# Optimization experiments

Hardware: AMD Instinct MI355X
Metric: run time of the kernel (lower is better)

Reference implementation:

```python
import jax, jax.numpy as jnp
import numpy as np

M = 4096          # number of quadrature points
D_OBS = 64        # number of observation directions
KVALS = (0.5, 1.0, 1.5, 2.0)   # wavenumbers (init k_values)
N_ITER = 5        # Born iterations
C = 1.0 / (4.0 * np.pi)        # Green's function constant


def setup_inputs() -> dict:
    key = jax.random.key(0)
    k1, k2, k3, k4 = jax.random.split(key, 4)
    pts = jax.random.normal(k1, (M, 3), dtype=jnp.float32)
    weights = jax.random.uniform(k2, (M,), dtype=jnp.float32)
    V = jax.random.normal(k3, (M,), dtype=jnp.float32)
    obs_dirs = jax.random.normal(k4, (D_OBS, 3), dtype=jnp.float32)
    obs_dirs = obs_dirs / jnp.linalg.norm(obs_dirs, axis=1, keepdims=True)
    return {"V": V, "obs_dirs": obs_dirs, "pts": pts, "weights": weights}


def reference(V, obs_dirs, pts, weights):
    dtype = V.dtype
    dhat = jnp.array([0.0, 0.0, 1.0], dtype=dtype)  # default incident_dir, already unit
    dot_d = pts @ dhat                               # [M]
    r2 = jnp.sum(pts * pts, axis=1)                  # [M]

    # Pairwise distances; faithful to D2 = r2_i + r2_j - 2 pts_i . pts_j
    D2 = r2[:, None] + r2[None, :] - 2.0 * (pts @ pts.T)   # [M, M]
    D = jnp.sqrt(jnp.clip(D2, 1e-12, None))
    invD = 1.0 / jnp.clip(D, 1e-6, None)
    idx = jnp.arange(M)
    invD = jnp.where(idx[:, None] == idx[None, :], jnp.zeros((), dtype), invD)
    scale = C * invD                                  # [M, M]

    VW = V * weights                                  # [M]
    Q = pts @ obs_dirs.T                              # [M, D_OBS]

    outs = []
    for k in KVALS:
        # Green's-function kernel (same across Born iterations for fixed k)
        Gr = scale * jnp.cos(k * D)                   # [M, M]
        Gi = scale * jnp.sin(k * D)                   # [M, M]

        # incident plane wave psi0 = exp(i k r.dhat)
        p0r = jnp.cos(k * dot_d)
        p0i = jnp.sin(k * dot_d)
        pr, pi_ = p0r, p0i
        for _ in range(N_ITER):
            ar = pr * VW
            ai = pi_ * VW
            pr = p0r + (Gr @ ar - Gi @ ai)
            pi_ = p0i + (Gr @ ai + Gi @ ar)

        # far-field amplitude: f(k, obs) = -C * sum_j w_j V_j psi_j exp(-i k pts_j.obs)
        phr = jnp.cos(-k * Q)                         # [M, D_OBS]
        phi = jnp.sin(-k * Q)
        zr = V * pr                                   # [M]
        zi = V * pi_
        ir = zr[:, None] * phr - zi[:, None] * phi    # [M, D_OBS]
        ii = zr[:, None] * phi + zi[:, None] * phr
        fr = jnp.sum(ir * weights[:, None], axis=0)   # [D_OBS]
        fi = jnp.sum(ii * weights[:, None], axis=0)
        outs.append(jnp.stack([-C * fr, -C * fi], axis=-1))  # [D_OBS, 2]

    return jnp.stack(outs, axis=0)                    # [len(KVALS), D_OBS, 2]
```

## Files before the change

### kernel.cpp

```cpp
#include <hip/hip_runtime.h>


#define MM 4096
#define NK 4
#define CGREEN 0.07957747154594767f

#define OFF_VW   49152
#define OFF_P0R  53248
#define OFF_P0I  69632
#define OFF_YR   86016
#define OFF_YI   102400
#define OFF_PART 118784
#define NCHUNK 128
#define PART_FLOATS (NCHUNK * 8 * MM)
#define WS_NEED_PART ((size_t)(OFF_PART + PART_FLOATS) * 4)

typedef float f2 __attribute__((ext_vector_type(2)));

__global__ __launch_bounds__(256) void init_k(const float* __restrict__ V,
                                              const float* __restrict__ pts,
                                              const float* __restrict__ w,
                                              float* __restrict__ ws) {
#pragma clang fp contract(off)
    int i = blockIdx.x * 256 + threadIdx.x;
    float x = pts[3 * i], y = pts[3 * i + 1], z = pts[3 * i + 2];
    float cvw = CGREEN * (V[i] * w[i]);
    float xx = x * x, yy = y * y, zz = z * z;
    float r2 = (xx + yy) + zz;
    float* cp = ws + i * 12;
    cp[0] = x; cp[1] = y; cp[2] = z; cp[3] = r2;
    ws[OFF_VW + i] = cvw;
#pragma unroll
    for (int n = 0; n < NK; n++) {
        float kk = 0.5f * (float)(n + 1);
        float s, c;
        sincosf(kk * z, &s, &c);
        ws[OFF_P0R + n * MM + i] = c;
        ws[OFF_P0I + n * MM + i] = s;
        cp[4 + n] = cvw * c;
        cp[8 + n] = cvw * s;
        ws[OFF_YR + n * MM + i] = 0.0f;
        ws[OFF_YI + n * MM + i] = 0.0f;
    }
}

__device__ __forceinline__ f2 cmul(f2 a, f2 b) {
    f2 r;
    r.x = fmaf(a.x, b.x, -(a.y * b.y));
    r.y = fmaf(a.x, b.y,  (a.y * b.x));
    return r;
}

__device__ __forceinline__ void body(float rx, float ry, float rz, float rr2,
                                     int rowg, int jg,
                                     float4 A, float4 R, float4 I,
                                     f2 acc[4]) {
    float d2;
    {
#pragma clang fp contract(off)
        float dot = fmaf(rz, A.z, fmaf(ry, A.y, rx * A.x));
        float r2s = rr2 + A.w;
        float twod = 2.0f * dot;
        d2 = r2s - twod;
    }
    d2 = fmaxf(d2, 1e-12f);
    float invD = __builtin_amdgcn_rsqf(d2);
    float D = d2 * invD;
    float scale = (rowg == jg) ? 0.0f : invD;
    float s1, c1;
    __sincosf(0.5f * D, &s1, &c1);
    f2 cs1 = {c1, s1};
    f2 cs2 = cmul(cs1, cs1);
    f2 cs3 = cmul(cs2, cs1);
    f2 cs4 = cmul(cs2, cs2);
    {
        f2 ri = {R.x, I.x}, sw = {-I.x, R.x};
        f2 t = cs1.x * ri; t += cs1.y * sw; acc[0] += scale * t;
    }
    {
        f2 ri = {R.y, I.y}, sw = {-I.y, R.y};
        f2 t = cs2.x * ri; t += cs2.y * sw; acc[1] += scale * t;
    }
    {
        f2 ri = {R.z, I.z}, sw = {-I.z, R.z};
        f2 t = cs3.x * ri; t += cs3.y * sw; acc[2] += scale * t;
    }
    {
        f2 ri = {R.w, I.w}, sw = {-I.w, R.w};
        f2 t = cs4.x * ri; t += cs4.y * sw; acc[3] += scale * t;
    }
}

template <int C, bool USE_PART>
__global__ __launch_bounds__(256) void matvec_k(float* __restrict__ ws) {
    constexpr int TC = MM / C;
    const int chunk = blockIdx.x;
    const int rg = blockIdx.y;
    const int r0 = rg * 256 + threadIdx.x;
    const float4 row0 = *(const float4*)&ws[r0 * 12];
    f2 acc[4];
#pragma unroll
    for (int i = 0; i < 4; i++) { acc[i].x = 0.0f; acc[i].y = 0.0f; }
    const int jg0 = chunk * TC;
    const float* colbase = ws + (size_t)jg0 * 12;
#pragma unroll 4
    for (int j = 0; j < TC; j++) {
        const float4* cp = (const float4*)(colbase + j * 12);
        float4 A = cp[0], R = cp[1], I = cp[2];
        body(row0.x, row0.y, row0.z, row0.w, r0, jg0 + j, A, R, I, acc);
    }
    if (USE_PART) {
        f2* part2 = (f2*)(ws + OFF_PART);
#pragma unroll
        for (int n = 0; n < NK; n++)
            part2[(size_t)(chunk * 4 + n) * MM + r0] = acc[n];
    } else {
        float* yr = ws + OFF_YR;
        float* yi = ws + OFF_YI;
#pragma unroll
        for (int n = 0; n < NK; n++) {
            atomicAdd(&yr[n * MM + r0], acc[n].x);
            atomicAdd(&yi[n * MM + r0], acc[n].y);
        }
    }
}

template <int C>
__global__ __launch_bounds__(64) void reduce_update_k(float* __restrict__ ws) {
    int tid = blockIdx.x * 64 + threadIdx.x;
    int row = tid & (MM - 1);
    int n = tid >> 12;
    const f2* part2 = (const f2*)(ws + OFF_PART);
    f2 s[8];
#pragma unroll
    for (int u = 0; u < 8; u++) { s[u].x = 0.0f; s[u].y = 0.0f; }
    for (int c = 0; c < C; c += 8) {
#pragma unroll
        for (int u = 0; u < 8; u++)
            s[u] += part2[(size_t)((c + u) * 4 + n) * MM + row];
    }
    f2 t = ((s[0] + s[1]) + (s[2] + s[3])) + ((s[4] + s[5]) + (s[6] + s[7]));
    float cvw = ws[OFF_VW + row];
    float pr = ws[OFF_P0R + n * MM + row] + t.x;
    float pi = ws[OFF_P0I + n * MM + row] + t.y;
    ws[row * 12 + 4 + n] = cvw * pr;
    ws[row * 12 + 8 + n] = cvw * pi;
}

__global__ __launch_bounds__(256) void update_fallback_k(float* __restrict__ ws) {
    int i = blockIdx.x * 256 + threadIdx.x;
    float cvw = ws[OFF_VW + i];
#pragma unroll
    for (int n = 0; n < NK; n++) {
        float pr = ws[OFF_P0R + n * MM + i] + ws[OFF_YR + n * MM + i];
        float pi = ws[OFF_P0I + n * MM + i] + ws[OFF_YI + n * MM + i];
        ws[i * 12 + 4 + n] = cvw * pr;
        ws[i * 12 + 8 + n] = cvw * pi;
        ws[OFF_YR + n * MM + i] = 0.0f;
        ws[OFF_YI + n * MM + i] = 0.0f;
    }
}

__global__ __launch_bounds__(256) void far_k(const float* __restrict__ obs,
                                             const float* __restrict__ ws,
                                             float* __restrict__ out) {
    int kidx = blockIdx.x >> 6;
    int d = blockIdx.x & 63;
    float kk = 0.5f * (float)(kidx + 1);
    float ox = obs[3 * d], oy = obs[3 * d + 1], oz = obs[3 * d + 2];
    float fr = 0.0f, fi = 0.0f;
    for (int j = threadIdx.x; j < MM; j += 256) {
        const float* c = ws + j * 12;
        float q = fmaf(c[2], oz, fmaf(c[1], oy, c[0] * ox));
        float ar = c[4 + kidx], ai = c[8 + kidx];
        float s, co;
        __sincosf(kk * q, &s, &co);
        fr += fmaf(ar, co,  ai * s);
        fi += fmaf(ai, co, -ar * s);
    }
#pragma unroll
    for (int off = 32; off > 0; off >>= 1) {
        fr += __shfl_down(fr, off);
        fi += __shfl_down(fi, off);
    }
    __shared__ float red[4][2];
    int wave = threadIdx.x >> 6;
    if ((threadIdx.x & 63) == 0) { red[wave][0] = fr; red[wave][1] = fi; }
    __syncthreads();
    if (threadIdx.x == 0) {
        fr = red[0][0] + red[1][0] + red[2][0] + red[3][0];
        fi = red[0][1] + red[1][1] + red[2][1] + red[3][1];
        out[(kidx * 64 + d) * 2 + 0] = -fr;
        out[(kidx * 64 + d) * 2 + 1] = -fi;
    }
}

extern "C" void kernel_launch(void* const* d_in, const int* in_sizes, int n_in,
                              void* d_out, int out_size, void* d_ws, size_t ws_size,
                              hipStream_t stream) {
    const float* V   = (const float*)d_in[0];
    const float* obs = (const float*)d_in[1];
    const float* pts = (const float*)d_in[2];
    const float* w   = (const float*)d_in[3];
    float* ws  = (float*)d_ws;
    float* out = (float*)d_out;

    init_k<<<16, 256, 0, stream>>>(V, pts, w, ws);
    if (ws_size >= WS_NEED_PART) {
        for (int it = 0; it < 5; it++) {
            matvec_k<NCHUNK, true><<<dim3(NCHUNK, 16), 256, 0, stream>>>(ws);
            reduce_update_k<NCHUNK><<<256, 64, 0, stream>>>(ws);
        }
    } else {
        for (int it = 0; it < 5; it++) {
            matvec_k<64, false><<<dim3(64, 16), 256, 0, stream>>>(ws);
            update_fallback_k<<<16, 256, 0, stream>>>(ws);
        }
    }
    far_k<<<256, 256, 0, stream>>>(obs, ws, out);
}
```

Baseline: 223.8 us.

## Process two rows per thread with packed f2 math and hardware sin/cos

Each matvec thread now handles two rows (r0 and r0+256), so every loaded column record is reused twice, and the grid is halved in the row dimension. Distance and harmonic computations are written in packed two-wide vectors so the compiler can emit packed FMA instructions. The sincos call is replaced by the raw hardware sin/cos builtins on a revolution-scaled argument. This cuts column loads and per-element instruction count, at the cost of more registers, fewer blocks, and possible accuracy loss from hardware sin/cos on larger arguments.

```diff
diff --git a/kernel.cpp b/kernel.cpp
--- a/kernel.cpp
+++ b/kernel.cpp
@@ -4,6 +4,7 @@
 #define MM 4096
 #define NK 4
 #define CGREEN 0.07957747154594767f
+#define INV2PI 0.15915494309189535f
 
 #define OFF_VW   49152
 #define OFF_P0R  53248
@@ -16,6 +17,10 @@
 #define WS_NEED_PART ((size_t)(OFF_PART + PART_FLOATS) * 4)
 
 typedef float f2 __attribute__((ext_vector_type(2)));
+
+__device__ __forceinline__ f2 vfma(f2 a, f2 b, f2 c) {
+    f2 r; r.x = fmaf(a.x, b.x, c.x); r.y = fmaf(a.y, b.y, c.y); return r;
+}
 
 __global__ __launch_bounds__(256) void init_k(const float* __restrict__ V,
                                               const float* __restrict__ pts,
@@ -44,83 +49,95 @@
     }
 }
 
-__device__ __forceinline__ f2 cmul(f2 a, f2 b) {
-    f2 r;
-    r.x = fmaf(a.x, b.x, -(a.y * b.y));
-    r.y = fmaf(a.x, b.y,  (a.y * b.x));
-    return r;
-}
-
-__device__ __forceinline__ void body(float rx, float ry, float rz, float rr2,
-                                     int rowg, int jg,
-                                     float4 A, float4 R, float4 I,
-                                     f2 acc[4]) {
-    float d2;
+__device__ __forceinline__ void body_col2(f2 rx, f2 ry, f2 rz, f2 rr2,
+                                          int r0, int r1, int jg,
+                                          float4 A, float4 R, float4 I,
+                                          f2 acc0[4], f2 acc1[4]) {
+    f2 d2;
     {
 #pragma clang fp contract(off)
-        float dot = fmaf(rz, A.z, fmaf(ry, A.y, rx * A.x));
-        float r2s = rr2 + A.w;
-        float twod = 2.0f * dot;
+        f2 m; m.x = rx.x * A.x; m.y = rx.y * A.x;
+        m = vfma(ry, (f2){A.y, A.y}, m);
+        m = vfma(rz, (f2){A.z, A.z}, m);
+        f2 r2s = rr2 + A.w;
+        f2 twod = 2.0f * m;
         d2 = r2s - twod;
     }
-    d2 = fmaxf(d2, 1e-12f);
-    float invD = __builtin_amdgcn_rsqf(d2);
-    float D = d2 * invD;
-    float scale = (rowg == jg) ? 0.0f : invD;
-    float s1, c1;
-    __sincosf(0.5f * D, &s1, &c1);
-    f2 cs1 = {c1, s1};
-    f2 cs2 = cmul(cs1, cs1);
-    f2 cs3 = cmul(cs2, cs1);
-    f2 cs4 = cmul(cs2, cs2);
-    {
-        f2 ri = {R.x, I.x}, sw = {-I.x, R.x};
-        f2 t = cs1.x * ri; t += cs1.y * sw; acc[0] += scale * t;
-    }
-    {
-        f2 ri = {R.y, I.y}, sw = {-I.y, R.y};
-        f2 t = cs2.x * ri; t += cs2.y * sw; acc[1] += scale * t;
-    }
-    {
-        f2 ri = {R.z, I.z}, sw = {-I.z, R.z};
-        f2 t = cs3.x * ri; t += cs3.y * sw; acc[2] += scale * t;
-    }
-    {
-        f2 ri = {R.w, I.w}, sw = {-I.w, R.w};
-        f2 t = cs4.x * ri; t += cs4.y * sw; acc[3] += scale * t;
-    }
+    d2.x = fmaxf(d2.x, 1e-12f);
+    d2.y = fmaxf(d2.y, 1e-12f);
+    float ia = __builtin_amdgcn_rsqf(d2.x);
+    float ib = __builtin_amdgcn_rsqf(d2.y);
+    f2 invD = {ia, ib};
+    f2 rev = d2 * invD * (0.5f * INV2PI);
+    float sca = (jg == r0) ? 0.0f : ia;
+    float scb = (jg == r1) ? 0.0f : ib;
+    f2 s1, c1;
+    s1.x = __builtin_amdgcn_sinf(rev.x);
+    c1.x = __builtin_amdgcn_cosf(rev.x);
+    s1.y = __builtin_amdgcn_sinf(rev.y);
+    c1.y = __builtin_amdgcn_cosf(rev.y);
+    f2 c2 = vfma(c1, c1, -(s1 * s1));
+    f2 s2 = 2.0f * (c1 * s1);
+    f2 c3 = vfma(c2, c1, -(s2 * s1));
+    f2 s3 = vfma(s2, c1, c2 * s1);
+    f2 c4 = vfma(c2, c2, -(s2 * s2));
+    f2 s4 = 2.0f * (c2 * s2);
+#define ACC_UPD(nn, CC, SS, ZR, ZI)                                          \
+    {                                                                        \
+        f2 ri = {ZR, ZI}, sw = {-ZI, ZR};                                    \
+        f2 t0 = CC.x * ri; t0 = vfma((f2){SS.x, SS.x}, sw, t0);              \
+        acc0[nn] = vfma((f2){sca, sca}, t0, acc0[nn]);                       \
+        f2 t1 = CC.y * ri; t1 = vfma((f2){SS.y, SS.y}, sw, t1);              \
+        acc1[nn] = vfma((f2){scb, scb}, t1, acc1[nn]);                       \
+    }
+    ACC_UPD(0, c1, s1, R.x, I.x)
+    ACC_UPD(1, c2, s2, R.y, I.y)
+    ACC_UPD(2, c3, s3, R.z, I.z)
+    ACC_UPD(3, c4, s4, R.w, I.w)
+#undef ACC_UPD
 }
 
 template <int C, bool USE_PART>
-__global__ __launch_bounds__(256) void matvec_k(float* __restrict__ ws) {
+__global__ __launch_bounds__(256) void matvec_k(const float* __restrict__ cols,
+                                                f2* __restrict__ part,
+                                                float* __restrict__ yr,
+                                                float* __restrict__ yi) {
     constexpr int TC = MM / C;
     const int chunk = blockIdx.x;
     const int rg = blockIdx.y;
-    const int r0 = rg * 256 + threadIdx.x;
-    const float4 row0 = *(const float4*)&ws[r0 * 12];
-    f2 acc[4];
-#pragma unroll
-    for (int i = 0; i < 4; i++) { acc[i].x = 0.0f; acc[i].y = 0.0f; }
+    const int r0 = rg * 512 + threadIdx.x;
+    const int r1 = r0 + 256;
+    const float4 rowA = *(const float4*)&cols[r0 * 12];
+    const float4 rowB = *(const float4*)&cols[r1 * 12];
+    const f2 rx = {rowA.x, rowB.x}, ry = {rowA.y, rowB.y};
+    const f2 rz = {rowA.z, rowB.z}, rr2 = {rowA.w, rowB.w};
+    f2 acc0[4], acc1[4];
+#pragma unroll
+    for (int i = 0; i < 4; i++) {
+        acc0[i].x = 0.0f; acc0[i].y = 0.0f;
+        acc1[i].x = 0.0f; acc1[i].y = 0.0f;
+    }
     const int jg0 = chunk * TC;
-    const float* colbase = ws + (size_t)jg0 * 12;
+    const float* colbase = cols + (size_t)jg0 * 12;
 #pragma unroll 4
     for (int j = 0; j < TC; j++) {
         const float4* cp = (const float4*)(colbase + j * 12);
         float4 A = cp[0], R = cp[1], I = cp[2];
-        body(row0.x, row0.y, row0.z, row0.w, r0, jg0 + j, A, R, I, acc);
+        body_col2(rx, ry, rz, rr2, r0, r1, jg0 + j, A, R, I, acc0, acc1);
     }
     if (USE_PART) {
-        f2* part2 = (f2*)(ws + OFF_PART);
-#pragma unroll
-        for (int n = 0; n < NK; n++)
-            part2[(size_t)(chunk * 4 + n) * MM + r0] = acc[n];
+#pragma unroll
+        for (int n = 0; n < NK; n++) {
+            part[(size_t)(chunk * 4 + n) * MM + r0] = acc0[n];
+            part[(size_t)(chunk * 4 + n) * MM + r1] = acc1[n];
+        }
     } else {
-        float* yr = ws + OFF_YR;
-        float* yi = ws + OFF_YI;
 #pragma unroll
         for (int n = 0; n < NK; n++) {
-            atomicAdd(&yr[n * MM + r0], acc[n].x);
-            atomicAdd(&yi[n * MM + r0], acc[n].y);
+            atomicAdd(&yr[n * MM + r0], acc0[n].x);
+            atomicAdd(&yi[n * MM + r0], acc0[n].y);
+            atomicAdd(&yr[n * MM + r1], acc1[n].x);
+            atomicAdd(&yi[n * MM + r1], acc1[n].y);
         }
     }
 }
@@ -208,12 +225,14 @@
     init_k<<<16, 256, 0, stream>>>(V, pts, w, ws);
     if (ws_size >= WS_NEED_PART) {
         for (int it = 0; it < 5; it++) {
-            matvec_k<NCHUNK, true><<<dim3(NCHUNK, 16), 256, 0, stream>>>(ws);
+            matvec_k<NCHUNK, true><<<dim3(NCHUNK, 8), 256, 0, stream>>>(
+                ws, (f2*)(ws + OFF_PART), ws + OFF_YR, ws + OFF_YI);
             reduce_update_k<NCHUNK><<<256, 64, 0, stream>>>(ws);
         }
     } else {
         for (int it = 0; it < 5; it++) {
-            matvec_k<64, false><<<dim3(64, 16), 256, 0, stream>>>(ws);
+            matvec_k<64, false><<<dim3(64, 8), 256, 0, stream>>>(
+                ws, (f2*)(ws + OFF_PART), ws + OFF_YR, ws + OFF_YI);
             update_fallback_k<<<16, 256, 0, stream>>>(ws);
         }
     }
```

After: 220.3 us. No clear change (-1.6%).
